# Kernel tuning notes

Measured on AMD Instinct MI355X. Metric: run time of the kernel, lower is better.

Reference implementation:

```python
import jax, jax.numpy as jnp
import numpy as np

N = 50000
E = 600000
D_IN = 128
D_HID = 128


def gcn_conv(x, src, dst, ew, W, b):
    """PyG-style GCNConv with self-loops and symmetric normalization.
    x: [N, Fin], src/dst: [E'], ew: [E'], W: [Fin, Fout], b: [Fout].
    """
    n = x.shape[0]
    # degree from incoming edge weights (self-loops already appended)
    deg = jax.ops.segment_sum(ew, dst, num_segments=n)
    dinv = jnp.where(deg > 0, jax.lax.rsqrt(deg), 0.0)
    norm = dinv[src] * ew * dinv[dst]  # [E']
    h = x @ W  # linear transform first (PyG order)
    msg = h[src] * norm[:, None]  # gather + scale, [E', Fout]
    out = jax.ops.segment_sum(msg, dst, num_segments=n)  # scatter-add
    return out + b


def setup_inputs() -> dict:
    key = jax.random.key(0)
    k1, k2, k3, k4, k5, k6, k7 = jax.random.split(key, 7)
    x = jax.random.normal(k1, (N, D_IN), dtype=jnp.float32)
    edge_index = jax.random.randint(k2, (2, E), 0, N, dtype=jnp.int64)
    edge_weight = jax.random.uniform(k3, (E,), dtype=jnp.float32)
    s1 = 1.0 / np.sqrt(D_IN)
    s2 = 1.0 / np.sqrt(D_HID)
    W1 = jax.random.uniform(k4, (D_IN, D_HID), dtype=jnp.float32, minval=-s1, maxval=s1)
    b1 = jax.random.uniform(k5, (D_HID,), dtype=jnp.float32, minval=-s1, maxval=s1)
    W2 = jax.random.uniform(k6, (D_HID, D_IN), dtype=jnp.float32, minval=-s2, maxval=s2)
    b2 = jax.random.uniform(k7, (D_IN,), dtype=jnp.float32, minval=-s2, maxval=s2)
    return {"x": x, "edge_index": edge_index, "edge_weight": edge_weight,
            "W1": W1, "b1": b1, "W2": W2, "b2": b2}


def reference(x, edge_index, edge_weight, W1, b1, W2, b2):
    n = x.shape[0]
    loops = jnp.arange(n, dtype=edge_index.dtype)
    src = jnp.concatenate([edge_index[0], loops])
    dst = jnp.concatenate([edge_index[1], loops])
    ew = jnp.concatenate([edge_weight, jnp.ones((n,), dtype=edge_weight.dtype)])
    h = gcn_conv(x, src, dst, ew, W1, b1)
    h = jax.nn.relu(h)
    h = gcn_conv(h, src, dst, ew, W2, b2)
    return jax.nn.sigmoid(h)
```

## Files before the change

kernel.cpp:

```cpp
#include <hip/hip_runtime.h>
#include <math.h>


typedef unsigned int uint32;
typedef unsigned long long u64;
typedef __attribute__((ext_vector_type(8))) short bf16x8;
typedef __attribute__((ext_vector_type(4))) float f32x4;
typedef __attribute__((ext_vector_type(2))) float f32x2;

__device__ __forceinline__ unsigned short f2bf(float f) {
    uint32 b = __float_as_uint(f);
    return (unsigned short)((b + 0x7FFFu + ((b >> 16) & 1u)) >> 16);
}

template <int AFP32, int OUTFP8>
__device__ __forceinline__ void gemm_body(const void* __restrict__ Ap,
                                          const unsigned short* __restrict__ WT,
                                          void* __restrict__ H,
                                          int n, int tb) {
    const int lane = threadIdx.x & 63;
    const int wv   = threadIdx.x >> 6;
    const int quad = lane >> 4;
    const int l16  = lane & 15;
    const int m0   = tb * 128 + wv * 32;
    f32x4 acc[2][8] = {};

    #pragma unroll
    for (int ks = 0; ks < 4; ++ks) {
        const int k0 = ks * 32 + quad * 8;
        bf16x8 a[2];
        #pragma unroll
        for (int rt = 0; rt < 2; ++rt) {
            int row = m0 + rt * 16 + l16;
            if (row >= n) row = n - 1;
            if (AFP32) {
                const float* Af = (const float*)Ap + (size_t)row * 128 + k0;
                float4 f0 = *(const float4*)(Af);
                float4 f1 = *(const float4*)(Af + 4);
                bf16x8 v;
                v[0] = (short)f2bf(f0.x); v[1] = (short)f2bf(f0.y);
                v[2] = (short)f2bf(f0.z); v[3] = (short)f2bf(f0.w);
                v[4] = (short)f2bf(f1.x); v[5] = (short)f2bf(f1.y);
                v[6] = (short)f2bf(f1.z); v[7] = (short)f2bf(f1.w);
                a[rt] = v;
            } else {
                const unsigned short* Ab = (const unsigned short*)Ap + (size_t)row * 128 + k0;
                a[rt] = *(const bf16x8*)Ab;
            }
        }
        #pragma unroll
        for (int ct = 0; ct < 8; ++ct) {
            bf16x8 b = *(const bf16x8*)(WT + (size_t)(ct * 16 + l16) * 128 + k0);
            acc[0][ct] = __builtin_amdgcn_mfma_f32_16x16x32_bf16(a[0], b, acc[0][ct], 0, 0, 0);
            acc[1][ct] = __builtin_amdgcn_mfma_f32_16x16x32_bf16(a[1], b, acc[1][ct], 0, 0, 0);
        }
    }

    #pragma unroll
    for (int rt = 0; rt < 2; ++rt) {
        #pragma unroll
        for (int r = 0; r < 4; ++r) {
            int row = m0 + rt * 16 + quad * 4 + r;
            if (row < n) {
                if (OUTFP8) {
                    unsigned char* o = (unsigned char*)H + (size_t)row * 128 + l16;
                    #pragma unroll
                    for (int cp = 0; cp < 4; ++cp) {
                        int pk = __builtin_amdgcn_cvt_pk_fp8_f32(
                            acc[rt][2 * cp][r], acc[rt][2 * cp + 1][r], 0, false);
                        o[(2 * cp) * 16]     = (unsigned char)(pk & 0xFF);
                        o[(2 * cp + 1) * 16] = (unsigned char)((pk >> 8) & 0xFF);
                    }
                } else {
                    unsigned short* o = (unsigned short*)H + (size_t)row * 128 + l16;
                    #pragma unroll
                    for (int ct = 0; ct < 8; ++ct)
                        o[ct * 16] = f2bf(acc[rt][ct][r]);
                }
            }
        }
    }
}

__global__ __launch_bounds__(256) void k_init(int* __restrict__ done,
                                              float2* __restrict__ csr, int E,
                                              const float* __restrict__ W1,
                                              const float* __restrict__ W2,
                                              unsigned short* __restrict__ WT1,
                                              unsigned short* __restrict__ WT2) {
    int idx = blockIdx.x * 256 + threadIdx.x;
    if (idx == 0) *done = 0;
    if (idx < 16) csr[E + idx] = make_float2(0.0f, 0.0f);
    int j = idx;
    int k = j >> 7, nn = j & 127;
    WT1[nn * 128 + k] = f2bf(W1[k * 128 + nn]);
    WT2[nn * 128 + k] = f2bf(W2[k * 128 + nn]);
}

__global__ __launch_bounds__(256) void k_gemm1_hist(const float* __restrict__ x,
                                                    const unsigned short* __restrict__ WT1,
                                                    unsigned char* __restrict__ h8,
                                                    const int* __restrict__ dst,
                                                    const float* __restrict__ ew,
                                                    u64* __restrict__ packed,
                                                    int* __restrict__ rank,
                                                    int E, int N, int gGemm) {
    const int b = blockIdx.x;
    if (b < gGemm) {
        gemm_body<1, 1>(x, WT1, h8, N, b);
        return;
    }
    int i = (b - gGemm) * 256 + threadIdx.x;
    if (i < E) {
        int d = dst[i];
        int r = (i >> 8) & 7;
        u64 add = (1ULL << 44) + (u64)(ew[i] * 4294967296.0f);
        u64 old = atomicAdd(&packed[(size_t)r * N + d], add);
        rank[i] = (int)(old >> 44);
    }
}

__global__ __launch_bounds__(256) void k_scan(const u64* __restrict__ packed,
                                              float* __restrict__ dinv,
                                              u64* __restrict__ bases,
                                              int* __restrict__ rowptr,
                                              int* __restrict__ csums,
                                              int* __restrict__ done, int nNodes) {
    __shared__ int s[256];
    __shared__ int lastFlag;
    const int t = threadIdx.x;
    const int base = blockIdx.x * 1024 + t * 4;
    const int n = nNodes + 1;
    int v[4];
    #pragma unroll
    for (int u = 0; u < 4; ++u) {
        int idx = base + u;
        int c = 0;
        if (idx < nNodes) {
            const u64 mask = (1ULL << 44) - 1;
            u64 ssum = 0;
            u64 bs = 0;
            uint32 cum = 0;
            #pragma unroll
            for (int r = 0; r < 8; ++r) {
                u64 pv = packed[(size_t)r * nNodes + idx];
                bs |= (u64)cum << (8 * r);
                cum += (uint32)(pv >> 44);
                ssum += (pv & mask);
            }
            c = (int)cum;
            float deg = 1.0f + (float)ssum * (1.0f / 4294967296.0f);
            dinv[idx] = rsqrtf(deg);
            bases[idx] = bs;
        }
        v[u] = c;
    }
    s[t] = v[0] + v[1] + v[2] + v[3];
    __syncthreads();
    #pragma unroll
    for (int off = 1; off < 256; off <<= 1) {
        int x = (t >= off) ? s[t - off] : 0;
        __syncthreads();
        s[t] += x;
        __syncthreads();
    }
    if (t == 255)
        __hip_atomic_store(&csums[blockIdx.x], s[255], __ATOMIC_RELEASE,
                           __HIP_MEMORY_SCOPE_AGENT);
    int e = (t == 0) ? 0 : s[t - 1];
    if (base + 0 < n) rowptr[base + 0] = e;
    if (base + 1 < n) rowptr[base + 1] = e + v[0];
    if (base + 2 < n) rowptr[base + 2] = e + v[0] + v[1];
    if (base + 3 < n) rowptr[base + 3] = e + v[0] + v[1] + v[2];

    __syncthreads();
    if (t == 0) {
        int prev = __hip_atomic_fetch_add(done, 1, __ATOMIC_ACQ_REL,
                                          __HIP_MEMORY_SCOPE_AGENT);
        lastFlag = (prev == (int)gridDim.x - 1);
    }
    __syncthreads();
    if (lastFlag && t < 64) {
        int g = (int)gridDim.x;
        int orig = (t < g) ? __hip_atomic_load(&csums[t], __ATOMIC_ACQUIRE,
                                               __HIP_MEMORY_SCOPE_AGENT)
                           : 0;
        int vv = orig;
        #pragma unroll
        for (int off = 1; off < 64; off <<= 1) {
            int y = __shfl_up(vv, off, 64);
            if (t >= off) vv += y;
        }
        if (t < g) csums[t] = vv - orig;
    }
}

__global__ __launch_bounds__(256) void k_fill(const int* __restrict__ src,
                                              const int* __restrict__ dst,
                                              const float* __restrict__ ew,
                                              const float* __restrict__ dinv,
                                              const int* __restrict__ rowptr,
                                              const int* __restrict__ csums,
                                              const u64* __restrict__ bases,
                                              const int* __restrict__ rank,
                                              float2* __restrict__ csr, int e) {
    int i = blockIdx.x * 256 + threadIdx.x;
    if (i < e) {
        int s = src[i], d = dst[i];
        int r = (i >> 8) & 7;
        float nrm = dinv[s] * ew[i] * dinv[d];
        int pos = rowptr[d] + csums[d >> 10]
                + (int)((bases[d] >> (8 * r)) & 0xFF) + rank[i];
        csr[pos] = make_float2(__int_as_float(s << 4), nrm);
    }
}

__device__ __forceinline__ void fma8_f8(float* acc, uint2 u, float w) {
    f32x2 f;
    f = __builtin_amdgcn_cvt_pk_f32_fp8((int)u.x, false);
    acc[0] += f[0] * w; acc[1] += f[1] * w;
    f = __builtin_amdgcn_cvt_pk_f32_fp8((int)u.x, true);
    acc[2] += f[0] * w; acc[3] += f[1] * w;
    f = __builtin_amdgcn_cvt_pk_f32_fp8((int)u.y, false);
    acc[4] += f[0] * w; acc[5] += f[1] * w;
    f = __builtin_amdgcn_cvt_pk_f32_fp8((int)u.y, true);
    acc[6] += f[0] * w; acc[7] += f[1] * w;
}

__device__ __forceinline__ void gather_q8p(float* acc, const uint2* __restrict__ T,
                                           const float2* __restrict__ csr,
                                           int start, int end, int l) {
    float2 c[8];
    #pragma unroll
    for (int j = 0; j < 8; ++j) c[j] = csr[start + j];
    for (int k = start; k < end; k += 8) {
        uint2 u[8];
        float w[8];
        float2 cn[8];
        #pragma unroll
        for (int j = 0; j < 8; ++j) {
            w[j] = (k + j < end) ? c[j].y : 0.0f;
            u[j] = T[(size_t)(uint32)__float_as_int(c[j].x) + l];
        }
        #pragma unroll
        for (int j = 0; j < 8; ++j) cn[j] = csr[k + 8 + j];
        #pragma unroll
        for (int j = 0; j < 8; ++j) fma8_f8(acc, u[j], w[j]);
        #pragma unroll
        for (int j = 0; j < 8; ++j) c[j] = cn[j];
    }
}

__global__ __launch_bounds__(256) void k_ag1(const unsigned char* __restrict__ h8,
                                             const float2* __restrict__ csr,
                                             const int* __restrict__ rowptr,
                                             const int* __restrict__ csums,
                                             const float* __restrict__ dinv,
                                             const float4* __restrict__ bias4,
                                             unsigned char* __restrict__ g8, int N) {
    const int lane = threadIdx.x & 63;
    const int q = lane >> 4, l = lane & 15;
    const int node = blockIdx.x * 16 + (threadIdx.x >> 6) * 4 + q;
    if (node >= N) return;
    const uint2* H2 = (const uint2*)h8;
    const int start = rowptr[node] + csums[node >> 10];
    const int end   = rowptr[node + 1] + csums[(node + 1) >> 10];
    const float di = dinv[node];

    float acc[8] = {};
    fma8_f8(acc, H2[(size_t)node * 16 + l], di * di);
    gather_q8p(acc, H2, csr, start, end, l);

    float4 b0 = bias4[l * 2], b1v = bias4[l * 2 + 1];
    acc[0] += b0.x;  acc[1] += b0.y;  acc[2] += b0.z;  acc[3] += b0.w;
    acc[4] += b1v.x; acc[5] += b1v.y; acc[6] += b1v.z; acc[7] += b1v.w;
    #pragma unroll
    for (int j = 0; j < 8; ++j) acc[j] = fmaxf(acc[j], 0.0f);
    uint2 o;
    int w0 = __builtin_amdgcn_cvt_pk_fp8_f32(acc[0], acc[1], 0, false);
    w0     = __builtin_amdgcn_cvt_pk_fp8_f32(acc[2], acc[3], w0, true);
    int w1 = __builtin_amdgcn_cvt_pk_fp8_f32(acc[4], acc[5], 0, false);
    w1     = __builtin_amdgcn_cvt_pk_fp8_f32(acc[6], acc[7], w1, true);
    o.x = (uint32)w0; o.y = (uint32)w1;
    ((uint2*)g8)[(size_t)node * 16 + l] = o;
}

__global__ __launch_bounds__(256) void k_ag2s(const unsigned char* __restrict__ g8,
                                              const float2* __restrict__ csr,
                                              const int* __restrict__ rowptr,
                                              const int* __restrict__ csums,
                                              const float* __restrict__ dinv,
                                              const float* __restrict__ b2,
                                              const unsigned short* __restrict__ WT2,
                                              float* __restrict__ out, int N) {
    __shared__ unsigned short sA[16][136];
    const int lane = threadIdx.x & 63;
    const int wv   = threadIdx.x >> 6;
    const int q    = lane >> 4;
    const int l    = lane & 15;
    const int nb   = blockIdx.x * 16;
    const int node = nb + wv * 4 + q;
    const uint2* G2 = (const uint2*)g8;

    float acc[8] = {};
    if (node < N) {
        const int start = rowptr[node] + csums[node >> 10];
        const int end   = rowptr[node + 1] + csums[(node + 1) >> 10];
        const float di = dinv[node];
        fma8_f8(acc, G2[(size_t)node * 16 + l], di * di);
        gather_q8p(acc, G2, csr, start, end, l);
    }
    uint4 o = make_uint4(0u, 0u, 0u, 0u);
    if (node < N) {
        o.x = (uint32)f2bf(acc[0]) | ((uint32)f2bf(acc[1]) << 16);
        o.y = (uint32)f2bf(acc[2]) | ((uint32)f2bf(acc[3]) << 16);
        o.z = (uint32)f2bf(acc[4]) | ((uint32)f2bf(acc[5]) << 16);
        o.w = (uint32)f2bf(acc[6]) | ((uint32)f2bf(acc[7]) << 16);
    }
    *(uint4*)&sA[wv * 4 + q][l * 8] = o;

    __syncthreads();

    f32x4 a2[2] = {};
    #pragma unroll
    for (int ks = 0; ks < 4; ++ks) {
        const int k0 = ks * 32 + q * 8;
        bf16x8 a = *(const bf16x8*)&sA[l][k0];
        #pragma unroll
        for (int ct = 0; ct < 2; ++ct) {
            bf16x8 b = *(const bf16x8*)(WT2 + (size_t)(wv * 32 + ct * 16 + l) * 128 + k0);
            a2[ct] = __builtin_amdgcn_mfma_f32_16x16x32_bf16(a, b, a2[ct], 0, 0, 0);
        }
    }
    #pragma unroll
    for (int ct = 0; ct < 2; ++ct) {
        const int col = wv * 32 + ct * 16 + l;
        const float bb = b2[col];
        #pragma unroll
        for (int r = 0; r < 4; ++r) {
            int row = nb + q * 4 + r;
            if (row < N) {
                float v = a2[ct][r] + bb;
                out[(size_t)row * 128 + col] = 1.0f / (1.0f + expf(-v));
            }
        }
    }
}

extern "C" void kernel_launch(void* const* d_in, const int* in_sizes, int n_in,
                              void* d_out, int out_size, void* d_ws, size_t ws_size,
                              hipStream_t stream) {
    const float* x  = (const float*)d_in[0];
    const int*   ei = (const int*)d_in[1];
    const float* ew = (const float*)d_in[2];
    const float* W1 = (const float*)d_in[3];
    const float* b1 = (const float*)d_in[4];
    const float* W2 = (const float*)d_in[5];
    const float* b2 = (const float*)d_in[6];

    const int N = in_sizes[0] / 128;
    const int E = in_sizes[2];
    const int* src = ei;
    const int* dst = ei + E;
    float* out = (float*)d_out;

    auto align = [](size_t v) { return (v + 255) & ~(size_t)255; };
    char* p = (char*)d_ws;
    float*  dinv   = (float*)p;   p += align((size_t)N * 4);
    int*    rowptr = (int*)p;     p += align((size_t)(N + 1) * 4);
    int*    csums  = (int*)p;     p += align((size_t)1024 * 4);
    int*    done   = (int*)p;     p += align((size_t)256);
    u64*    bases  = (u64*)p;     p += align((size_t)N * 8);
    unsigned short* WT1 = (unsigned short*)p; p += align((size_t)128 * 128 * 2);
    unsigned short* WT2 = (unsigned short*)p; p += align((size_t)128 * 128 * 2);
    int*    rank   = (int*)p;     p += align((size_t)E * 4);
    float2* csr    = (float2*)p;  p += align((size_t)(E + 16) * 8);
    unsigned char*  h8 = (unsigned char*)p;  p += align((size_t)N * 128);
    unsigned char*  g8 = (unsigned char*)p;
    u64* packed = (u64*)g8;

    const int nbE = (E + 255) / 256;
    const int gScan = (N + 1 + 1023) / 1024;
    const int gGemm = (N + 127) / 128;
    const int gAg1  = (N + 15) / 16;
    const int gAg2  = (N + 15) / 16;

    hipMemsetAsync(packed, 0, (size_t)N * 8 * 8, stream);
    k_init<<<64, 256, 0, stream>>>(done, csr, E, W1, W2, WT1, WT2);
    k_gemm1_hist<<<gGemm + nbE, 256, 0, stream>>>(x, WT1, h8, dst, ew, packed,
                                                  rank, E, N, gGemm);
    k_scan<<<gScan, 256, 0, stream>>>(packed, dinv, bases, rowptr, csums, done, N);
    k_fill<<<nbE, 256, 0, stream>>>(src, dst, ew, dinv, rowptr, csums, bases,
                                    rank, csr, E);

    k_ag1<<<gAg1, 256, 0, stream>>>(h8, csr, rowptr, csums, dinv,
                                    (const float4*)b1, g8, N);

    k_ag2s<<<gAg2, 256, 0, stream>>>(g8, csr, rowptr, csums, dinv, b2,
                                     WT2, out, N);
}
```

Measured before the change: 193.2 us.

## Split aggregation by feature half with XCC-aware work queue, separate GEMM2

Each aggregation block now processes one 64-feature half of 16 nodes. Blocks take work from an atomic queue keyed by the XCC id, so each XCC tends to stay on one half of the feature table and its L2 holds a smaller working set. Layer 2 writes bf16 aggregates to a buffer, and a separate full-tile MFMA GEMM with sigmoid replaces the fused per-16-node GEMM. The cost is an extra kernel launch, an extra write and read of the intermediate, and duplicated CSR index reads across the two halves. The workspace layout is also reordered so agg2 reuses the h8 region.

```diff
diff --git a/kernel.cpp b/kernel.cpp
--- a/kernel.cpp
+++ b/kernel.cpp
@@ -83,6 +83,7 @@
 }
 
 __global__ __launch_bounds__(256) void k_init(int* __restrict__ done,
+                                              int* __restrict__ qctr,
                                               float2* __restrict__ csr, int E,
                                               const float* __restrict__ W1,
                                               const float* __restrict__ W2,
@@ -90,9 +91,9 @@
                                               unsigned short* __restrict__ WT2) {
     int idx = blockIdx.x * 256 + threadIdx.x;
     if (idx == 0) *done = 0;
+    if (idx < 4) qctr[idx] = 0;
     if (idx < 16) csr[E + idx] = make_float2(0.0f, 0.0f);
-    int j = idx;
-    int k = j >> 7, nn = j & 127;
+    int k = idx >> 7, nn = idx & 127;
     WT1[nn * 128 + k] = f2bf(W1[k * 128 + nn]);
     WT2[nn * 128 + k] = f2bf(W2[k * 128 + nn]);
 }
@@ -215,40 +216,49 @@
     }
 }
 
-__device__ __forceinline__ void fma8_f8(float* acc, uint2 u, float w) {
+__device__ __forceinline__ void fma4_f8(float* acc, uint32 u, float w) {
     f32x2 f;
-    f = __builtin_amdgcn_cvt_pk_f32_fp8((int)u.x, false);
+    f = __builtin_amdgcn_cvt_pk_f32_fp8((int)u, false);
     acc[0] += f[0] * w; acc[1] += f[1] * w;
-    f = __builtin_amdgcn_cvt_pk_f32_fp8((int)u.x, true);
+    f = __builtin_amdgcn_cvt_pk_f32_fp8((int)u, true);
     acc[2] += f[0] * w; acc[3] += f[1] * w;
-    f = __builtin_amdgcn_cvt_pk_f32_fp8((int)u.y, false);
-    acc[4] += f[0] * w; acc[5] += f[1] * w;
-    f = __builtin_amdgcn_cvt_pk_f32_fp8((int)u.y, true);
-    acc[6] += f[0] * w; acc[7] += f[1] * w;
-}
-
-__device__ __forceinline__ void gather_q8p(float* acc, const uint2* __restrict__ T,
+}
+
+__device__ __forceinline__ void gather_h8p(float* acc, const uint32* __restrict__ T,
                                            const float2* __restrict__ csr,
-                                           int start, int end, int l) {
+                                           int start, int end, int cbase) {
     float2 c[8];
     #pragma unroll
     for (int j = 0; j < 8; ++j) c[j] = csr[start + j];
     for (int k = start; k < end; k += 8) {
-        uint2 u[8];
+        uint32 u[8];
         float w[8];
         float2 cn[8];
         #pragma unroll
         for (int j = 0; j < 8; ++j) {
             w[j] = (k + j < end) ? c[j].y : 0.0f;
-            u[j] = T[(size_t)(uint32)__float_as_int(c[j].x) + l];
+            u[j] = T[(((size_t)(uint32)__float_as_int(c[j].x)) << 1) + cbase];
         }
         #pragma unroll
         for (int j = 0; j < 8; ++j) cn[j] = csr[k + 8 + j];
         #pragma unroll
-        for (int j = 0; j < 8; ++j) fma8_f8(acc, u[j], w[j]);
+        for (int j = 0; j < 8; ++j) fma4_f8(acc, u[j], w[j]);
         #pragma unroll
         for (int j = 0; j < 8; ++j) c[j] = cn[j];
     }
+}
+
+__device__ __forceinline__ void pop_work(int* __restrict__ qctr, int ngroups,
+                                         int* sH, int* sG) {
+    if (threadIdx.x == 0) {
+        uint32 xcc;
+        asm volatile("s_getreg_b32 %0, hwreg(HW_REG_XCC_ID)" : "=s"(xcc));
+        int h = (int)(xcc & 1u);
+        int g = atomicAdd(&qctr[h], 1);
+        if (g >= ngroups) { h ^= 1; g = atomicAdd(&qctr[h], 1); }
+        *sH = h; *sG = g;
+    }
+    __syncthreads();
 }
 
 __global__ __launch_bounds__(256) void k_ag1(const unsigned char* __restrict__ h8,
@@ -257,91 +267,109 @@
                                              const int* __restrict__ csums,
                                              const float* __restrict__ dinv,
                                              const float4* __restrict__ bias4,
-                                             unsigned char* __restrict__ g8, int N) {
+                                             unsigned char* __restrict__ g8,
+                                             int* __restrict__ qctr,
+                                             int ngroups, int N) {
+    __shared__ int sH, sG;
+    pop_work(qctr, ngroups, &sH, &sG);
+    const int half = sH, grp = sG;
+    if (grp >= ngroups) return;
     const int lane = threadIdx.x & 63;
     const int q = lane >> 4, l = lane & 15;
-    const int node = blockIdx.x * 16 + (threadIdx.x >> 6) * 4 + q;
+    const int node = grp * 16 + (threadIdx.x >> 6) * 4 + q;
     if (node >= N) return;
-    const uint2* H2 = (const uint2*)h8;
+    const uint32* H1 = (const uint32*)h8;
+    const int cbase = half * 16 + l;
     const int start = rowptr[node] + csums[node >> 10];
     const int end   = rowptr[node + 1] + csums[(node + 1) >> 10];
     const float di = dinv[node];
 
-    float acc[8] = {};
-    fma8_f8(acc, H2[(size_t)node * 16 + l], di * di);
-    gather_q8p(acc, H2, csr, start, end, l);
-
-    float4 b0 = bias4[l * 2], b1v = bias4[l * 2 + 1];
-    acc[0] += b0.x;  acc[1] += b0.y;  acc[2] += b0.z;  acc[3] += b0.w;
-    acc[4] += b1v.x; acc[5] += b1v.y; acc[6] += b1v.z; acc[7] += b1v.w;
-    #pragma unroll
-    for (int j = 0; j < 8; ++j) acc[j] = fmaxf(acc[j], 0.0f);
-    uint2 o;
+    float acc[4] = {};
+    fma4_f8(acc, H1[(size_t)node * 32 + cbase], di * di);
+    gather_h8p(acc, H1, csr, start, end, cbase);
+
+    float4 bb = bias4[cbase];
+    acc[0] += bb.x; acc[1] += bb.y; acc[2] += bb.z; acc[3] += bb.w;
+    #pragma unroll
+    for (int j = 0; j < 4; ++j) acc[j] = fmaxf(acc[j], 0.0f);
     int w0 = __builtin_amdgcn_cvt_pk_fp8_f32(acc[0], acc[1], 0, false);
     w0     = __builtin_amdgcn_cvt_pk_fp8_f32(acc[2], acc[3], w0, true);
-    int w1 = __builtin_amdgcn_cvt_pk_fp8_f32(acc[4], acc[5], 0, false);
-    w1     = __builtin_amdgcn_cvt_pk_fp8_f32(acc[6], acc[7], w1, true);
-    o.x = (uint32)w0; o.y = (uint32)w1;
-    ((uint2*)g8)[(size_t)node * 16 + l] = o;
-}
-
-__global__ __launch_bounds__(256) void k_ag2s(const unsigned char* __restrict__ g8,
-                                              const float2* __restrict__ csr,
-                                              const int* __restrict__ rowptr,
-                                              const int* __restrict__ csums,
-                                              const float* __restrict__ dinv,
-                                              const float* __restrict__ b2,
-                                              const unsigned short* __restrict__ WT2,
-                                              float* __restrict__ out, int N) {
-    __shared__ unsigned short sA[16][136];
+    ((uint32*)g8)[(size_t)node * 32 + cbase] = (uint32)w0;
+}
+
+__global__ __launch_bounds__(256) void k_ag2(const unsigned char* __restrict__ g8,
+                                             const float2* __restrict__ csr,
+                                             const int* __restrict__ rowptr,
+                                             const int* __restrict__ csums,
+                                             const float* __restrict__ dinv,
+                                             unsigned short* __restrict__ agg2,
+                                             int* __restrict__ qctr,
+                                             int ngroups, int N) {
+    __shared__ int sH, sG;
+    pop_work(qctr, ngroups, &sH, &sG);
+    const int half = sH, grp = sG;
+    if (grp >= ngroups) return;
+    const int lane = threadIdx.x & 63;
+    const int q = lane >> 4, l = lane & 15;
+    const int node = grp * 16 + (threadIdx.x >> 6) * 4 + q;
+    if (node >= N) return;
+    const uint32* G1 = (const uint32*)g8;
+    const int cbase = half * 16 + l;
+    const int start = rowptr[node] + csums[node >> 10];
+    const int end   = rowptr[node + 1] + csums[(node + 1) >> 10];
+    const float di = dinv[node];
+
+    float acc[4] = {};
+    fma4_f8(acc, G1[(size_t)node * 32 + cbase], di * di);
+    gather_h8p(acc, G1, csr, start, end, cbase);
+
+    uint2 o;
+    o.x = (uint32)f2bf(acc[0]) | ((uint32)f2bf(acc[1]) << 16);
+    o.y = (uint32)f2bf(acc[2]) | ((uint32)f2bf(acc[3]) << 16);
+    ((uint2*)agg2)[(size_t)node * 32 + cbase] = o;
+}
+
+__global__ __launch_bounds__(256) void k_gemm2s(const unsigned short* __restrict__ A,
+                                                const unsigned short* __restrict__ WT2,
+                                                const float* __restrict__ b2,
+                                                float* __restrict__ out, int n) {
     const int lane = threadIdx.x & 63;
     const int wv   = threadIdx.x >> 6;
-    const int q    = lane >> 4;
-    const int l    = lane & 15;
-    const int nb   = blockIdx.x * 16;
-    const int node = nb + wv * 4 + q;
-    const uint2* G2 = (const uint2*)g8;
-
-    float acc[8] = {};
-    if (node < N) {
-        const int start = rowptr[node] + csums[node >> 10];
-        const int end   = rowptr[node + 1] + csums[(node + 1) >> 10];
-        const float di = dinv[node];
-        fma8_f8(acc, G2[(size_t)node * 16 + l], di * di);
-        gather_q8p(acc, G2, csr, start, end, l);
-    }
-    uint4 o = make_uint4(0u, 0u, 0u, 0u);
-    if (node < N) {
-        o.x = (uint32)f2bf(acc[0]) | ((uint32)f2bf(acc[1]) << 16);
-        o.y = (uint32)f2bf(acc[2]) | ((uint32)f2bf(acc[3]) << 16);
-        o.z = (uint32)f2bf(acc[4]) | ((uint32)f2bf(acc[5]) << 16);
-        o.w = (uint32)f2bf(acc[6]) | ((uint32)f2bf(acc[7]) << 16);
-    }
-    *(uint4*)&sA[wv * 4 + q][l * 8] = o;
-
-    __syncthreads();
-
-    f32x4 a2[2] = {};
+    const int quad = lane >> 4;
+    const int l16  = lane & 15;
+    const int m0   = blockIdx.x * 128 + wv * 32;
+    f32x4 acc[2][8] = {};
+
     #pragma unroll
     for (int ks = 0; ks < 4; ++ks) {
-        const int k0 = ks * 32 + q * 8;
-        bf16x8 a = *(const bf16x8*)&sA[l][k0];
-        #pragma unroll
-        for (int ct = 0; ct < 2; ++ct) {
-            bf16x8 b = *(const bf16x8*)(WT2 + (size_t)(wv * 32 + ct * 16 + l) * 128 + k0);
-            a2[ct] = __builtin_amdgcn_mfma_f32_16x16x32_bf16(a, b, a2[ct], 0, 0, 0);
-        }
-    }
-    #pragma unroll
-    for (int ct = 0; ct < 2; ++ct) {
-        const int col = wv * 32 + ct * 16 + l;
-        const float bb = b2[col];
+        const int k0 = ks * 32 + quad * 8;
+        bf16x8 a[2];
+        #pragma unroll
+        for (int rt = 0; rt < 2; ++rt) {
+            int row = m0 + rt * 16 + l16;
+            if (row >= n) row = n - 1;
+            a[rt] = *(const bf16x8*)(A + (size_t)row * 128 + k0);
+        }
+        #pragma unroll
+        for (int ct = 0; ct < 8; ++ct) {
+            bf16x8 b = *(const bf16x8*)(WT2 + (size_t)(ct * 16 + l16) * 128 + k0);
+            acc[0][ct] = __builtin_amdgcn_mfma_f32_16x16x32_bf16(a[0], b, acc[0][ct], 0, 0, 0);
+            acc[1][ct] = __builtin_amdgcn_mfma_f32_16x16x32_bf16(a[1], b, acc[1][ct], 0, 0, 0);
+        }
+    }
+
+    #pragma unroll
+    for (int rt = 0; rt < 2; ++rt) {
         #pragma unroll
         for (int r = 0; r < 4; ++r) {
-            int row = nb + q * 4 + r;
-            if (row < N) {
-                float v = a2[ct][r] + bb;
-                out[(size_t)row * 128 + col] = 1.0f / (1.0f + expf(-v));
+            int row = m0 + rt * 16 + quad * 4 + r;
+            if (row < n) {
+                #pragma unroll
+                for (int ct = 0; ct < 8; ++ct) {
+                    int col = ct * 16 + l16;
+                    float v = acc[rt][ct][r] + b2[col];
+                    out[(size_t)row * 128 + col] = 1.0f / (1.0f + expf(-v));
+                }
             }
         }
     }
@@ -370,32 +398,36 @@
     int*    rowptr = (int*)p;     p += align((size_t)(N + 1) * 4);
     int*    csums  = (int*)p;     p += align((size_t)1024 * 4);
     int*    done   = (int*)p;     p += align((size_t)256);
+    int*    qctr   = (int*)p;     p += align((size_t)256);
     u64*    bases  = (u64*)p;     p += align((size_t)N * 8);
     unsigned short* WT1 = (unsigned short*)p; p += align((size_t)128 * 128 * 2);
     unsigned short* WT2 = (unsigned short*)p; p += align((size_t)128 * 128 * 2);
+    float2* csr    = (float2*)p;  p += align((size_t)(E + 16) * 8);
+    unsigned char*  g8 = (unsigned char*)p;  p += align((size_t)N * 128);
+    unsigned char*  h8 = (unsigned char*)p;
+    unsigned short* agg2 = (unsigned short*)h8;
+    p += align((size_t)N * 128);
     int*    rank   = (int*)p;     p += align((size_t)E * 4);
-    float2* csr    = (float2*)p;  p += align((size_t)(E + 16) * 8);
-    unsigned char*  h8 = (unsigned char*)p;  p += align((size_t)N * 128);
-    unsigned char*  g8 = (unsigned char*)p;
     u64* packed = (u64*)g8;
 
     const int nbE = (E + 255) / 256;
     const int gScan = (N + 1 + 1023) / 1024;
     const int gGemm = (N + 127) / 128;
-    const int gAg1  = (N + 15) / 16;
-    const int gAg2  = (N + 15) / 16;
+    const int ngroups = (N + 15) / 16;
+    const int gAgg = 2 * ngroups;
 
     hipMemsetAsync(packed, 0, (size_t)N * 8 * 8, stream);
-    k_init<<<64, 256, 0, stream>>>(done, csr, E, W1, W2, WT1, WT2);
+    k_init<<<64, 256, 0, stream>>>(done, qctr, csr, E, W1, W2, WT1, WT2);
     k_gemm1_hist<<<gGemm + nbE, 256, 0, stream>>>(x, WT1, h8, dst, ew, packed,
                                                   rank, E, N, gGemm);
     k_scan<<<gScan, 256, 0, stream>>>(packed, dinv, bases, rowptr, csums, done, N);
     k_fill<<<nbE, 256, 0, stream>>>(src, dst, ew, dinv, rowptr, csums, bases,
                                     rank, csr, E);
 
-    k_ag1<<<gAg1, 256, 0, stream>>>(h8, csr, rowptr, csums, dinv,
-                                    (const float4*)b1, g8, N);
-
-    k_ag2s<<<gAg2, 256, 0, stream>>>(g8, csr, rowptr, csums, dinv, b2,
-                                     WT2, out, N);
-}
+    k_ag1<<<gAgg, 256, 0, stream>>>(h8, csr, rowptr, csums, dinv,
+                                    (const float4*)b1, g8, qctr, ngroups, N);
+
+    k_ag2<<<gAgg, 256, 0, stream>>>(g8, csr, rowptr, csums, dinv, agg2,
+                                    qctr + 2, ngroups, N);
+    k_gemm2s<<<gGemm, 256, 0, stream>>>(agg2, WT2, b2, out, N);
+}
```

New measurement: 318.9 us. 65.1% more time.
